# Optimization experiments

Hardware: AMD Instinct MI355X
Metric: run time of the kernel (lower is better)

## Reference

```python
import jax, jax.numpy as jnp
import numpy as np

S_DIM = 4096
N_NODES = 4096
N_EDGES = 32768


def _coarsen(ei_np, N):
    """Integer-only greedy coarsening, faithful to MNGRAPH.forward's while-loop.
    Returns (select order, flattened neighbor indices, segment ids, per-hub
    neighbor counts, forward-fill indices replicating the stale-M behavior for
    empty neighborhoods, and the remapped final edge_index)."""
    ei = ei_np.astype(np.int64).copy()
    I = np.bincount(ei[0], minlength=N)
    O = np.bincount(ei[1], minlength=N)
    order = np.argsort(-(I + O), kind='stable')  # torch.argsort(D, descending=True)
    visits = np.zeros(N, dtype=bool)
    select = []
    nbr_idx, nbr_seg, counts = [], [], []
    while order.size > 0:
        node = int(order[0])
        select.append(node)
        visits[node] = True
        # H = unique neighbors of node in the CURRENT (rewritten) edge_index
        H = np.unique(np.concatenate([ei[1][ei[0] == node], ei[0][ei[1] == node]]))
        visits[H] = True
        order = order[~visits[order]]
        # rewrite: endpoints in H that are not already-selected hubs -> node
        Hn = H[~np.isin(H, np.asarray(select, dtype=np.int64))]
        ei[np.isin(ei, Hn)] = node
        ei = ei[:, ei[0] != ei[1]]  # drop self-loops
        # append reversed edges that are not already present (pair-code isin
        # == the original O(E^2) all/any comparison, computed efficiently)
        code = ei[0] * N + ei[1]
        rcode = ei[1] * N + ei[0]
        new = ~np.isin(rcode, code)
        ei = np.concatenate([ei, ei[::-1][:, new]], axis=1)
        k = len(select) - 1
        nbr_idx.append(H)
        nbr_seg.append(np.full(H.shape[0], k, dtype=np.int64))
        counts.append(H.shape[0])
    select = np.asarray(select, dtype=np.int64)
    sort_sel = np.sort(select)
    ei_out = np.searchsorted(sort_sel, ei)  # compact node ids
    counts = np.asarray(counts, dtype=np.int64)
    # forward-fill: when H is empty the original appends the previous (stale) M
    fill = np.arange(select.shape[0])
    for i in range(select.shape[0]):
        if counts[i] == 0:
            fill[i] = fill[i - 1] if i > 0 else 0
    nbr = np.concatenate(nbr_idx) if nbr_idx else np.zeros(0, np.int64)
    seg = np.concatenate(nbr_seg) if nbr_seg else np.zeros(0, np.int64)
    return select, nbr, seg, counts, fill, ei_out


def setup_inputs() -> dict:
    key = jax.random.key(0)
    k1, k2, k3, k4 = jax.random.split(key, 4)
    x = jax.random.normal(k1, (N_NODES, S_DIM), dtype=jnp.float32)
    edge_index = jax.random.randint(k2, (2, N_EDGES), 0, N_NODES, dtype=jnp.int64)
    bound = float(np.sqrt(6.0 / (1.0 + S_DIM)))  # xavier_uniform on (1, S)
    W1 = jax.random.uniform(k3, (S_DIM,), jnp.float32, -bound, bound)
    W2 = jax.random.uniform(k4, (S_DIM,), jnp.float32, -bound, bound)
    B1 = jnp.zeros((S_DIM,), jnp.float32)
    B2 = jnp.zeros((S_DIM,), jnp.float32)
    return {"x": x, "edge_index": edge_index, "W1": W1, "W2": W2, "B1": B1, "B2": B2}


def reference(x, edge_index, W1, W2, B1, B2):
    N = x.shape[0]
    sel, nbr, seg, counts, fill, ei_out = _coarsen(np.asarray(edge_index), N)
    K = sel.shape[0]
    # Dn = x[n]*W1+B1 for every neighbor of every hub; per-hub mean via segment_sum
    Dn = x[jnp.asarray(nbr)] * W1 + B1                      # [T, S]
    sums = jax.ops.segment_sum(Dn, jnp.asarray(seg), num_segments=K)
    denom = jnp.maximum(jnp.asarray(counts), 1).astype(x.dtype)[:, None]
    mean_Dn = sums / denom                                  # [K, S]
    Dv = x[jnp.asarray(sel)] * W2 + B2                      # [K, S]
    END = jnp.concatenate([Dv, mean_Dn], axis=1)            # [K, 2S]
    END = END[jnp.asarray(fill)]                            # stale-M replication
    return END, jnp.asarray(ei_out)
```

## Files before the change

kernel.cpp:

```cpp
#include <hip/hip_runtime.h>
#include <hip/hip_bf16.h>

#define NT 1024
#define NNODES 4096
#define ECAP 65536

__device__ __forceinline__ int blockScanExcl(int v, int* s_w, int* total) {
    const int tid  = threadIdx.x;
    const int lane = tid & 63;
    const int wv   = tid >> 6;
    int x = v;
#pragma unroll
    for (int off = 1; off < 64; off <<= 1) {
        int t = __shfl_up(x, off, 64);
        if (lane >= off) x += t;
    }
    if (lane == 63) s_w[wv] = x;
    __syncthreads();
    if (tid < 16) {
        int y = s_w[tid];
#pragma unroll
        for (int off = 1; off < 16; off <<= 1) {
            int t = __shfl_up(y, off, 16);
            if (tid >= off) y += t;
        }
        s_w[tid] = y;
    }
    __syncthreads();
    int base = wv ? s_w[wv - 1] : 0;
    int tot  = s_w[15];
    __syncthreads();
    *total = tot;
    return base + x - v;
}

__global__ __launch_bounds__(NT, 1)
void phaseA(const int* __restrict__ ei, int E0,
            int* __restrict__ U, int* __restrict__ V,
            unsigned int* __restrict__ BM,
            int* __restrict__ NBR, int* __restrict__ OTH, int* __restrict__ TMP,
            int* __restrict__ SEL, int* __restrict__ CNTS,
            int* __restrict__ NST, int* __restrict__ FIL, int* __restrict__ SC,
            float* __restrict__ out)
{
    __shared__ unsigned short s_order[NNODES];
    __shared__ unsigned char  s_vis[NNODES];
    __shared__ unsigned char  s_sel[NNODES];
    __shared__ unsigned int   s_hb[NNODES / 32];
    __shared__ unsigned short s_so[NNODES];
    __shared__ unsigned int   s_nst[NNODES + 1];
    __shared__ int s_roff[NNODES];
    __shared__ int s_rend[NNODES];
    __shared__ int s_tmp[NNODES];
    __shared__ unsigned short s_lab[NNODES];
    __shared__ int s_stamp[NNODES];
    __shared__ int s_w[16];
    __shared__ int s_bc[16];

    const int tid = threadIdx.x;
    const int ln  = tid & 63;

    for (int i = tid; i < NNODES; i += NT) {
        s_vis[i] = 0; s_sel[i] = 0; s_tmp[i] = 0; s_stamp[i] = 0;
    }
    for (int i = tid; i < NNODES / 32; i += NT) s_hb[i] = 0;
    if (tid < 16) s_bc[tid] = 0;
    __syncthreads();

    for (int i = tid; i < E0; i += NT)
        if (ei[2 * i + 1] != 0) s_bc[9] = 1;
    __syncthreads();
    const int is64 = !s_bc[9];

    for (int e = tid; e < E0; e += NT) {
        int uu = ei[is64 ? 2 * e : e];
        int vv = ei[is64 ? 2 * (E0 + e) : (E0 + e)];
        U[e] = uu; V[e] = vv;
        atomicAdd(&s_tmp[uu], 1);
        atomicAdd(&s_tmp[vv], 1);
    }
    __syncthreads();
    for (int n = tid; n < NNODES; n += NT) atomicMax(&s_bc[7], s_tmp[n]);
    __syncthreads();
    const int maxd = s_bc[7];

    for (int d = maxd; d >= 0; --d) {
        int n0 = tid * 4;
        int f0 = (s_tmp[n0] == d), f1 = (s_tmp[n0 + 1] == d);
        int f2 = (s_tmp[n0 + 2] == d), f3 = (s_tmp[n0 + 3] == d);
        int tot;
        int off = blockScanExcl(f0 + f1 + f2 + f3, s_w, &tot);
        int idx = s_bc[4] + off;
        if (f0) s_order[idx++] = (unsigned short)n0;
        if (f1) s_order[idx++] = (unsigned short)(n0 + 1);
        if (f2) s_order[idx++] = (unsigned short)(n0 + 2);
        if (f3) s_order[idx++] = (unsigned short)(n0 + 3);
        __syncthreads();
        if (tid == 0) s_bc[4] += tot;
        __syncthreads();
    }

    if (tid == 0) {
        int nd = s_order[0];
        s_bc[0] = nd; s_sel[nd] = 1; s_vis[nd] = 1;
        s_so[0] = (unsigned short)nd; s_nst[0] = 0;
    }
    __syncthreads();
    {
        const int node = s_bc[0];
        for (int e = tid; e < E0; e += NT) {
            int uu = U[e], vv = V[e];
            if (uu == node) {
                int w = vv; unsigned m = 1u << (w & 31);
                unsigned old = atomicOr(&s_hb[w >> 5], m);
                if (!(old & m)) { int i = atomicAdd(&s_bc[2], 1); s_tmp[i] = w; s_vis[w] = 1; }
            }
            if (vv == node) {
                int w = uu; unsigned m = 1u << (w & 31);
                unsigned old = atomicOr(&s_hb[w >> 5], m);
                if (!(old & m)) { int i = atomicAdd(&s_bc[2], 1); s_tmp[i] = w; s_vis[w] = 1; }
            }
        }
        __syncthreads();
        for (int e = tid; e < E0; e += NT) {
            int uu = U[e];
            if (uu != node && ((s_hb[uu >> 5] >> (uu & 31)) & 1)) U[e] = node;
            int vv = V[e];
            if (vv != node && ((s_hb[vv >> 5] >> (vv & 31)) & 1)) V[e] = node;
        }
        __syncthreads();
    }

    for (int i = tid; i < (1 << 19); i += NT) BM[i] = 0u;
    __syncthreads();
    for (int e = tid; e < E0; e += NT) {
        int uu = U[e], vv = V[e];
        if (uu != vv) {
            unsigned code = ((unsigned)uu << 12) | (unsigned)vv;
            atomicOr(&BM[code >> 5], 1u << (code & 31));
        }
    }
    __syncthreads();
    for (int t = 0; t < E0; t += NT) {
        int e = t + tid, flag = 0, uu = 0, vv = 0;
        if (e < E0) {
            uu = U[e]; vv = V[e];
            if (uu != vv) {
                unsigned rc = ((unsigned)vv << 12) | (unsigned)uu;
                unsigned old = atomicOr(&BM[rc >> 5], 0u);
                flag = !((old >> (rc & 31)) & 1u);
            }
        }
        int tot;
        int off = blockScanExcl(flag, s_w, &tot);
        if (flag) { int r = s_bc[5] + off; U[E0 + r] = vv; V[E0 + r] = uu; }
        __syncthreads();
        if (tid == 0) s_bc[5] += tot;
        __syncthreads();
    }
    const int E1 = E0 + s_bc[5];

    for (int n = tid; n < NNODES; n += NT) s_roff[n] = 0;
    __syncthreads();
    for (int e = tid; e < E1; e += NT) {
        int uu = U[e], vv = V[e];
        if (uu != vv) { atomicAdd(&s_roff[uu], 1); atomicAdd(&s_roff[vv], 1); }
    }
    __syncthreads();
    {
        int n0 = tid * 4;
        int c0 = s_roff[n0], c1 = s_roff[n0 + 1], c2 = s_roff[n0 + 2], c3 = s_roff[n0 + 3];
        int tot;
        int off = blockScanExcl(c0 + c1 + c2 + c3, s_w, &tot);
        int st = off;
        s_roff[n0] = st;     s_rend[n0] = st;     st += c0;
        s_roff[n0 + 1] = st; s_rend[n0 + 1] = st; st += c1;
        s_roff[n0 + 2] = st; s_rend[n0 + 2] = st; st += c2;
        s_roff[n0 + 3] = st; s_rend[n0 + 3] = st;
    }
    __syncthreads();
    for (int e = tid; e < E1; e += NT) {
        int uu = U[e], vv = V[e];
        if (uu != vv) {
            int p = atomicAdd(&s_rend[uu], 1);
            int q = atomicAdd(&s_rend[vv], 1);
            OTH[p] = vv; OTH[q] = uu;
        }
    }
    __syncthreads();
    {
        const int cnt0 = s_bc[2];
        for (int i = tid; i < cnt0; i += NT) NBR[i] = s_tmp[i];
    }
    for (int i = tid; i < NNODES; i += NT) s_lab[i] = (unsigned short)i;
    __syncthreads();

    int p = 0, k = 1;
    for (;;) {
        __syncthreads();
        if (tid == 0) s_nst[k] = (unsigned)s_bc[2];
        int node = -1;
        for (;;) {
            if (p >= NNODES) break;
            int cand = (p + ln < NNODES) ? (int)s_order[p + ln] : -1;
            int unvis = (cand >= 0) && (!s_vis[cand]);
            unsigned long long bal = __ballot(unvis);
            if (bal != 0ull) {
                int sel = __ffsll(bal) - 1;
                node = __shfl(cand, sel, 64);
                p += sel + 1;
                break;
            }
            p += 64;
        }
        if (node < 0) break;
        if (tid == 0) { s_sel[node] = 1; s_so[k] = (unsigned short)node; }
        const int rb = s_roff[node], re = s_rend[node];
        for (int s = rb + tid; s < re; s += NT) {
            int w = (int)s_lab[OTH[s]];
            if (w == node) continue;
            int old = atomicMax(&s_stamp[w], k);
            if (old < k) {
                int i = atomicAdd(&s_bc[2], 1);
                NBR[i] = w;
                s_vis[w] = 1;
                if (!s_sel[w]) s_lab[w] = (unsigned short)node;
            }
        }
        k++;
    }
    const int K = k;
    __syncthreads();

    for (int i = tid; i < K; i += NT) {
        SEL[i]  = (int)s_so[i];
        CNTS[i] = (int)(s_nst[i + 1] - s_nst[i]);
        NST[i]  = (int)s_nst[i];
    }
    if (tid == 0) {
        SC[0] = K;
        int f = 0;
        for (int i = 0; i < K; i++) { if (s_nst[i + 1] > s_nst[i]) f = i; FIL[i] = f; }
    }
    {
        int n0 = tid * 4;
        int r0 = s_sel[n0], r1 = s_sel[n0 + 1], r2 = s_sel[n0 + 2], r3 = s_sel[n0 + 3];
        int tot;
        int off = blockScanExcl(r0 + r1 + r2 + r3, s_w, &tot);
        int st = off;
        s_tmp[n0] = st;     st += r0;
        s_tmp[n0 + 1] = st; st += r1;
        s_tmp[n0 + 2] = st; st += r2;
        s_tmp[n0 + 3] = st;
    }
    __syncthreads();
    const size_t obase = (size_t)K * 8192;
    for (int t = 0; t < E1; t += NT) {
        int e = t + tid, flag = 0, ru = 0, rv = 0;
        if (e < E1) {
            int uu = (int)s_lab[U[e]], vv = (int)s_lab[V[e]];
            if (uu != vv) { flag = 1; ru = s_tmp[uu]; rv = s_tmp[vv]; }
        }
        int tot;
        int off = blockScanExcl(flag, s_w, &tot);
        if (flag) {
            int r = s_bc[6] + off;
            out[obase + (size_t)r] = (float)ru;
            TMP[r] = rv;
        }
        __syncthreads();
        if (tid == 0) s_bc[6] += tot;
        __syncthreads();
    }
    const int Ef = s_bc[6];
    if (tid == 0) SC[1] = Ef;
    for (int r = tid; r < Ef; r += NT)
        out[obase + (size_t)Ef + (size_t)r] = (float)TMP[r];
}

__global__ __launch_bounds__(256, 4)
void phaseB(const float* __restrict__ x,
            const float* __restrict__ W1, const float* __restrict__ W2,
            const float* __restrict__ B1, const float* __restrict__ B2,
            const int* __restrict__ NBR, const int* __restrict__ SEL,
            const int* __restrict__ CNTS, const int* __restrict__ NST,
            const int* __restrict__ FIL, const int* __restrict__ SC,
            float* __restrict__ out)
{
    const int K = SC[0];
    const int k = blockIdx.x;
    if (k >= K) return;
    const int kk   = FIL[k];
    const int node = SEL[kk];
    const int cnt  = CNTS[kk];
    const int st   = NST[kk];
    const int tid  = threadIdx.x;
    const float4* x4 = (const float4*)x;

    float4 acc[4];
#pragma unroll
    for (int j = 0; j < 4; j++) acc[j] = make_float4(0.f, 0.f, 0.f, 0.f);

    for (int r = 0; r < cnt; ++r) {
        const float4* row = x4 + (size_t)NBR[st + r] * 1024;
#pragma unroll
        for (int j = 0; j < 4; j++) {
            float4 t = row[tid + j * 256];
            acc[j].x += t.x; acc[j].y += t.y; acc[j].z += t.z; acc[j].w += t.w;
        }
    }

    const float fc  = (float)cnt;
    const float inv = 1.0f / (float)(cnt > 1 ? cnt : 1);
    const float4* xr = x4 + (size_t)node * 1024;
    float4* o4 = (float4*)(out + (size_t)k * 8192);

#pragma unroll
    for (int j = 0; j < 4; j++) {
        int c = tid + j * 256;
        float4 w1 = ((const float4*)W1)[c], b1 = ((const float4*)B1)[c];
        float4 w2 = ((const float4*)W2)[c], b2 = ((const float4*)B2)[c];
        float4 xv = xr[c];
        float4 pd, pm;
        pd.x = xv.x * w2.x + b2.x;
        pd.y = xv.y * w2.y + b2.y;
        pd.z = xv.z * w2.z + b2.z;
        pd.w = xv.w * w2.w + b2.w;
        pm.x = (acc[j].x * w1.x + fc * b1.x) * inv;
        pm.y = (acc[j].y * w1.y + fc * b1.y) * inv;
        pm.z = (acc[j].z * w1.z + fc * b1.z) * inv;
        pm.w = (acc[j].w * w1.w + fc * b1.w) * inv;
        o4[c] = pd;
        o4[1024 + c] = pm;
    }
}

extern "C" void kernel_launch(void* const* d_in, const int* in_sizes, int n_in,
                              void* d_out, int out_size, void* d_ws, size_t ws_size,
                              hipStream_t stream)
{
    const float* x  = (const float*)d_in[0];
    const int*   ei = (const int*)d_in[1];
    const float* W1 = (const float*)d_in[2];
    const float* W2 = (const float*)d_in[3];
    const float* B1 = (const float*)d_in[4];
    const float* B2 = (const float*)d_in[5];
    const int E0 = in_sizes[1] / 2;

    char* w = (char*)d_ws;
    int* U = (int*)w;
    int* V = U + ECAP;
    unsigned int* BM = (unsigned int*)(V + ECAP);
    int* OTH = (int*)BM;
    int* NBR = OTH + 2 * ECAP;
    int* TMP = NBR + 2 * ECAP;
    char* meta = (char*)BM + (2u << 20);
    int* SEL  = (int*)meta;
    int* CNTS = SEL + NNODES;
    int* NST  = CNTS + NNODES;
    int* FIL  = NST + NNODES;
    int* SC   = FIL + NNODES;
    float* out = (float*)d_out;

    hipLaunchKernelGGL(phaseA, dim3(1), dim3(NT), 0, stream,
                       ei, E0, U, V, BM, NBR, OTH, TMP,
                       SEL, CNTS, NST, FIL, SC, out);
    hipLaunchKernelGGL(phaseB, dim3(NNODES), dim3(256), 0, stream,
                       x, W1, W2, B1, B2, NBR, SEL, CNTS, NST, FIL, SC, out);
}
```

Measured before the change: 972.5 us.

## Cut barriers in serial coarsening loop via per-wave atomics and chunked compaction

Packs the visited flag into the order array (high bit) with a position index, so the hub search reads one LDS array. Neighbor insertion now uses wave-aggregated atomics and per-hub counters, and the loop top uses a raw LDS-wait-plus-barrier instead of __syncthreads with a tid-0 write. The reverse-edge append and final edge compaction switch from per-tile scans with two barriers each to one block scan over per-thread contiguous chunks with bitmasks, dropping the TMP buffer. The bitmap clear is vectorised to uint4. The goal is to remove synchronisation and atomic overhead in the single-block serial phase. The cost is extra LDS and a 64-bit mask assumption that requires each thread's chunk to be at most 64 edges.

```diff
diff --git a/kernel.cpp b/kernel.cpp
--- a/kernel.cpp
+++ b/kernel.cpp
@@ -4,6 +4,8 @@
 #define NT 1024
 #define NNODES 4096
 #define ECAP 65536
+
+#define BAR_LDS() asm volatile("s_waitcnt lgkmcnt(0)\n\ts_barrier" ::: "memory")
 
 __device__ __forceinline__ int blockScanExcl(int v, int* s_w, int* total) {
     const int tid  = threadIdx.x;
@@ -38,17 +40,17 @@
 void phaseA(const int* __restrict__ ei, int E0,
             int* __restrict__ U, int* __restrict__ V,
             unsigned int* __restrict__ BM,
-            int* __restrict__ NBR, int* __restrict__ OTH, int* __restrict__ TMP,
+            int* __restrict__ NBR, int* __restrict__ OTH,
             int* __restrict__ SEL, int* __restrict__ CNTS,
             int* __restrict__ NST, int* __restrict__ FIL, int* __restrict__ SC,
             float* __restrict__ out)
 {
-    __shared__ unsigned short s_order[NNODES];
-    __shared__ unsigned char  s_vis[NNODES];
+    __shared__ unsigned short s_ordvis[NNODES];
+    __shared__ unsigned short s_pos[NNODES];
     __shared__ unsigned char  s_sel[NNODES];
     __shared__ unsigned int   s_hb[NNODES / 32];
     __shared__ unsigned short s_so[NNODES];
-    __shared__ unsigned int   s_nst[NNODES + 1];
+    __shared__ int s_cnt32[NNODES];
     __shared__ int s_roff[NNODES];
     __shared__ int s_rend[NNODES];
     __shared__ int s_tmp[NNODES];
@@ -61,7 +63,7 @@
     const int ln  = tid & 63;
 
     for (int i = tid; i < NNODES; i += NT) {
-        s_vis[i] = 0; s_sel[i] = 0; s_tmp[i] = 0; s_stamp[i] = 0;
+        s_sel[i] = 0; s_tmp[i] = 0; s_stamp[i] = 0; s_cnt32[i] = 0;
     }
     for (int i = tid; i < NNODES / 32; i += NT) s_hb[i] = 0;
     if (tid < 16) s_bc[tid] = 0;
@@ -91,19 +93,22 @@
         int tot;
         int off = blockScanExcl(f0 + f1 + f2 + f3, s_w, &tot);
         int idx = s_bc[4] + off;
-        if (f0) s_order[idx++] = (unsigned short)n0;
-        if (f1) s_order[idx++] = (unsigned short)(n0 + 1);
-        if (f2) s_order[idx++] = (unsigned short)(n0 + 2);
-        if (f3) s_order[idx++] = (unsigned short)(n0 + 3);
+        if (f0) s_ordvis[idx++] = (unsigned short)n0;
+        if (f1) s_ordvis[idx++] = (unsigned short)(n0 + 1);
+        if (f2) s_ordvis[idx++] = (unsigned short)(n0 + 2);
+        if (f3) s_ordvis[idx++] = (unsigned short)(n0 + 3);
         __syncthreads();
         if (tid == 0) s_bc[4] += tot;
         __syncthreads();
     }
+    for (int i = tid; i < NNODES; i += NT) s_pos[(int)s_ordvis[i]] = (unsigned short)i;
+    __syncthreads();
 
     if (tid == 0) {
-        int nd = s_order[0];
-        s_bc[0] = nd; s_sel[nd] = 1; s_vis[nd] = 1;
-        s_so[0] = (unsigned short)nd; s_nst[0] = 0;
+        int nd = (int)s_ordvis[0];
+        s_bc[0] = nd; s_sel[nd] = 1;
+        s_ordvis[0] = (unsigned short)(0x8000 | nd);
+        s_so[0] = (unsigned short)nd;
     }
     __syncthreads();
     {
@@ -113,15 +118,22 @@
             if (uu == node) {
                 int w = vv; unsigned m = 1u << (w & 31);
                 unsigned old = atomicOr(&s_hb[w >> 5], m);
-                if (!(old & m)) { int i = atomicAdd(&s_bc[2], 1); s_tmp[i] = w; s_vis[w] = 1; }
+                if (!(old & m)) {
+                    int i = atomicAdd(&s_bc[2], 1); s_tmp[i] = w;
+                    s_ordvis[s_pos[w]] = (unsigned short)(0x8000 | w);
+                }
             }
             if (vv == node) {
                 int w = uu; unsigned m = 1u << (w & 31);
                 unsigned old = atomicOr(&s_hb[w >> 5], m);
-                if (!(old & m)) { int i = atomicAdd(&s_bc[2], 1); s_tmp[i] = w; s_vis[w] = 1; }
+                if (!(old & m)) {
+                    int i = atomicAdd(&s_bc[2], 1); s_tmp[i] = w;
+                    s_ordvis[s_pos[w]] = (unsigned short)(0x8000 | w);
+                }
             }
         }
         __syncthreads();
+        if (tid == 0) s_cnt32[0] = s_bc[2];
         for (int e = tid; e < E0; e += NT) {
             int uu = U[e];
             if (uu != node && ((s_hb[uu >> 5] >> (uu & 31)) & 1)) U[e] = node;
@@ -131,7 +143,10 @@
         __syncthreads();
     }
 
-    for (int i = tid; i < (1 << 19); i += NT) BM[i] = 0u;
+    {
+        uint4* bm4 = (uint4*)BM;
+        for (int i = tid; i < (1 << 17); i += NT) bm4[i] = make_uint4(0, 0, 0, 0);
+    }
     __syncthreads();
     for (int e = tid; e < E0; e += NT) {
         int uu = U[e], vv = V[e];
@@ -141,24 +156,32 @@
         }
     }
     __syncthreads();
-    for (int t = 0; t < E0; t += NT) {
-        int e = t + tid, flag = 0, uu = 0, vv = 0;
-        if (e < E0) {
-            uu = U[e]; vv = V[e];
-            if (uu != vv) {
-                unsigned rc = ((unsigned)vv << 12) | (unsigned)uu;
-                unsigned old = atomicOr(&BM[rc >> 5], 0u);
-                flag = !((old >> (rc & 31)) & 1u);
+    int E1;
+    {
+        const int chA = (E0 + NT - 1) / NT;
+        const int begA = tid * chA;
+        unsigned long long mA = 0ull;
+        for (int j = 0; j < chA; ++j) {
+            int e = begA + j;
+            if (e < E0) {
+                int uu = U[e], vv = V[e];
+                if (uu != vv) {
+                    unsigned rc = ((unsigned)vv << 12) | (unsigned)uu;
+                    unsigned old = atomicOr(&BM[rc >> 5], 0u);
+                    if (!((old >> (rc & 31)) & 1u)) mA |= 1ull << j;
+                }
             }
         }
         int tot;
-        int off = blockScanExcl(flag, s_w, &tot);
-        if (flag) { int r = s_bc[5] + off; U[E0 + r] = vv; V[E0 + r] = uu; }
-        __syncthreads();
-        if (tid == 0) s_bc[5] += tot;
-        __syncthreads();
-    }
-    const int E1 = E0 + s_bc[5];
+        int off = blockScanExcl(__popcll(mA), s_w, &tot);
+        for (int j = 0; j < chA; ++j) if ((mA >> j) & 1) {
+            int e = begA + j;
+            int r = off++;
+            U[E0 + r] = V[e]; V[E0 + r] = U[e];
+        }
+        E1 = E0 + tot;
+    }
+    __syncthreads();
 
     for (int n = tid; n < NNODES; n += NT) s_roff[n] = 0;
     __syncthreads();
@@ -197,17 +220,15 @@
 
     int p = 0, k = 1;
     for (;;) {
-        __syncthreads();
-        if (tid == 0) s_nst[k] = (unsigned)s_bc[2];
+        BAR_LDS();
         int node = -1;
-        for (;;) {
-            if (p >= NNODES) break;
-            int cand = (p + ln < NNODES) ? (int)s_order[p + ln] : -1;
-            int unvis = (cand >= 0) && (!s_vis[cand]);
-            unsigned long long bal = __ballot(unvis);
+        while (p < NNODES) {
+            int idx = p + ln;
+            int ov = (idx < NNODES) ? (int)s_ordvis[idx] : 0x8000;
+            unsigned long long bal = __ballot(!(ov & 0x8000));
             if (bal != 0ull) {
                 int sel = __ffsll(bal) - 1;
-                node = __shfl(cand, sel, 64);
+                node = __shfl(ov, sel, 64) & 0x7FFF;
                 p += sel + 1;
                 break;
             }
@@ -216,15 +237,31 @@
         if (node < 0) break;
         if (tid == 0) { s_sel[node] = 1; s_so[k] = (unsigned short)node; }
         const int rb = s_roff[node], re = s_rend[node];
-        for (int s = rb + tid; s < re; s += NT) {
-            int w = (int)s_lab[OTH[s]];
-            if (w == node) continue;
-            int old = atomicMax(&s_stamp[w], k);
-            if (old < k) {
-                int i = atomicAdd(&s_bc[2], 1);
-                NBR[i] = w;
-                s_vis[w] = 1;
-                if (!s_sel[w]) s_lab[w] = (unsigned short)node;
+        for (int s0 = rb; s0 < re; s0 += NT) {
+            int s = s0 + tid;
+            bool isnew = false; int w = -1;
+            if (s < re) {
+                w = (int)s_lab[OTH[s]];
+                if (w != node) {
+                    int old = atomicMax(&s_stamp[w], k);
+                    isnew = old < k;
+                }
+            }
+            unsigned long long b = __ballot(isnew);
+            if (b != 0ull) {
+                int cnt = __popcll(b);
+                int before = __popcll(b & ((1ull << ln) - 1ull));
+                int base = 0;
+                if (isnew && before == 0) {
+                    base = atomicAdd(&s_bc[2], cnt);
+                    atomicAdd(&s_cnt32[k], cnt);
+                }
+                base = __shfl(base, __ffsll(b) - 1, 64);
+                if (isnew) {
+                    NBR[base + before] = w;
+                    s_ordvis[s_pos[w]] = (unsigned short)(0x8000 | w);
+                    if (!s_sel[w]) s_lab[w] = (unsigned short)node;
+                }
             }
         }
         k++;
@@ -232,15 +269,24 @@
     const int K = k;
     __syncthreads();
 
-    for (int i = tid; i < K; i += NT) {
-        SEL[i]  = (int)s_so[i];
-        CNTS[i] = (int)(s_nst[i + 1] - s_nst[i]);
-        NST[i]  = (int)s_nst[i];
-    }
+    {
+        int n0 = tid * 4;
+        int c0 = s_cnt32[n0], c1 = s_cnt32[n0 + 1], c2 = s_cnt32[n0 + 2], c3 = s_cnt32[n0 + 3];
+        int tot;
+        int off = blockScanExcl(c0 + c1 + c2 + c3, s_w, &tot);
+        if (n0 < K) {
+            int st = off;
+            if (n0     < K) { NST[n0]     = st; CNTS[n0]     = c0; } st += c0;
+            if (n0 + 1 < K) { NST[n0 + 1] = st; CNTS[n0 + 1] = c1; } st += c1;
+            if (n0 + 2 < K) { NST[n0 + 2] = st; CNTS[n0 + 2] = c2; } st += c2;
+            if (n0 + 3 < K) { NST[n0 + 3] = st; CNTS[n0 + 3] = c3; }
+        }
+    }
+    for (int i = tid; i < K; i += NT) SEL[i] = (int)s_so[i];
     if (tid == 0) {
         SC[0] = K;
         int f = 0;
-        for (int i = 0; i < K; i++) { if (s_nst[i + 1] > s_nst[i]) f = i; FIL[i] = f; }
+        for (int i = 0; i < K; i++) { if (s_cnt32[i] > 0) f = i; FIL[i] = f; }
     }
     {
         int n0 = tid * 4;
@@ -254,28 +300,29 @@
         s_tmp[n0 + 3] = st;
     }
     __syncthreads();
-    const size_t obase = (size_t)K * 8192;
-    for (int t = 0; t < E1; t += NT) {
-        int e = t + tid, flag = 0, ru = 0, rv = 0;
-        if (e < E1) {
-            int uu = (int)s_lab[U[e]], vv = (int)s_lab[V[e]];
-            if (uu != vv) { flag = 1; ru = s_tmp[uu]; rv = s_tmp[vv]; }
-        }
-        int tot;
-        int off = blockScanExcl(flag, s_w, &tot);
-        if (flag) {
-            int r = s_bc[6] + off;
-            out[obase + (size_t)r] = (float)ru;
-            TMP[r] = rv;
-        }
-        __syncthreads();
-        if (tid == 0) s_bc[6] += tot;
-        __syncthreads();
-    }
-    const int Ef = s_bc[6];
-    if (tid == 0) SC[1] = Ef;
-    for (int r = tid; r < Ef; r += NT)
-        out[obase + (size_t)Ef + (size_t)r] = (float)TMP[r];
+    {
+        const int ch2 = (E1 + NT - 1) / NT;
+        const int beg2 = tid * ch2;
+        unsigned long long mF = 0ull;
+        for (int j = 0; j < ch2; ++j) {
+            int e = beg2 + j;
+            if (e < E1) {
+                int uu = (int)s_lab[U[e]], vv = (int)s_lab[V[e]];
+                if (uu != vv) mF |= 1ull << j;
+            }
+        }
+        int Ef;
+        int off = blockScanExcl(__popcll(mF), s_w, &Ef);
+        const size_t obase = (size_t)K * 8192;
+        int r = off;
+        for (int j = 0; j < ch2; ++j) if ((mF >> j) & 1) {
+            int e = beg2 + j;
+            out[obase + (size_t)r]             = (float)s_tmp[(int)s_lab[U[e]]];
+            out[obase + (size_t)Ef + (size_t)r] = (float)s_tmp[(int)s_lab[V[e]]];
+            r++;
+        }
+        if (tid == 0) SC[1] = Ef;
+    }
 }
 
 __global__ __launch_bounds__(256, 4)
@@ -353,7 +400,6 @@
     unsigned int* BM = (unsigned int*)(V + ECAP);
     int* OTH = (int*)BM;
     int* NBR = OTH + 2 * ECAP;
-    int* TMP = NBR + 2 * ECAP;
     char* meta = (char*)BM + (2u << 20);
     int* SEL  = (int*)meta;
     int* CNTS = SEL + NNODES;
@@ -363,7 +409,7 @@
     float* out = (float*)d_out;
 
     hipLaunchKernelGGL(phaseA, dim3(1), dim3(NT), 0, stream,
-                       ei, E0, U, V, BM, NBR, OTH, TMP,
+                       ei, E0, U, V, BM, NBR, OTH,
                        SEL, CNTS, NST, FIL, SC, out);
     hipLaunchKernelGGL(phaseB, dim3(NNODES), dim3(256), 0, stream,
                        x, W1, W2, B1, B2, NBR, SEL, CNTS, NST, FIL, SC, out);
```

New measurement: 1.192 ms. +22.6%, slower.

## Split serial coarsening loop into single-wavefront kernel without block barriers

Applied to the files above, without the earlier changes.

The phaseA kernel is split into three kernels. The sequential greedy hub-selection loop now runs in one 64-thread wavefront, which removes the per-iteration __syncthreads across 1024 threads. The visited flags are folded into the order array so one ballot can find the next unvisited hub, and neighbors are processed two per lane. The exclusive scans and the forward fill use wave-level ballot and shuffle, the relabel pass runs in a separate 1024-thread kernel, and the extra launches pass their data through global memory.

```diff
diff --git a/kernel.cpp b/kernel.cpp
--- a/kernel.cpp
+++ b/kernel.cpp
@@ -35,34 +35,25 @@
 }
 
 __global__ __launch_bounds__(NT, 1)
-void phaseA(const int* __restrict__ ei, int E0,
-            int* __restrict__ U, int* __restrict__ V,
-            unsigned int* __restrict__ BM,
-            int* __restrict__ NBR, int* __restrict__ OTH, int* __restrict__ TMP,
-            int* __restrict__ SEL, int* __restrict__ CNTS,
-            int* __restrict__ NST, int* __restrict__ FIL, int* __restrict__ SC,
-            float* __restrict__ out)
+void phaseA1(const int* __restrict__ ei, int E0,
+             int* __restrict__ U, int* __restrict__ V,
+             unsigned int* __restrict__ BM,
+             int* __restrict__ NBR, int* __restrict__ OTH,
+             int* __restrict__ ORDV, int* __restrict__ ROFFG, int* __restrict__ RENDG,
+             int* __restrict__ HAND)
 {
     __shared__ unsigned short s_order[NNODES];
     __shared__ unsigned char  s_vis[NNODES];
-    __shared__ unsigned char  s_sel[NNODES];
     __shared__ unsigned int   s_hb[NNODES / 32];
-    __shared__ unsigned short s_so[NNODES];
-    __shared__ unsigned int   s_nst[NNODES + 1];
     __shared__ int s_roff[NNODES];
     __shared__ int s_rend[NNODES];
     __shared__ int s_tmp[NNODES];
-    __shared__ unsigned short s_lab[NNODES];
-    __shared__ int s_stamp[NNODES];
     __shared__ int s_w[16];
     __shared__ int s_bc[16];
 
     const int tid = threadIdx.x;
-    const int ln  = tid & 63;
-
-    for (int i = tid; i < NNODES; i += NT) {
-        s_vis[i] = 0; s_sel[i] = 0; s_tmp[i] = 0; s_stamp[i] = 0;
-    }
+
+    for (int i = tid; i < NNODES; i += NT) { s_vis[i] = 0; s_tmp[i] = 0; }
     for (int i = tid; i < NNODES / 32; i += NT) s_hb[i] = 0;
     if (tid < 16) s_bc[tid] = 0;
     __syncthreads();
@@ -102,8 +93,7 @@
 
     if (tid == 0) {
         int nd = s_order[0];
-        s_bc[0] = nd; s_sel[nd] = 1; s_vis[nd] = 1;
-        s_so[0] = (unsigned short)nd; s_nst[0] = 0;
+        s_bc[0] = nd; s_vis[nd] = 1;
     }
     __syncthreads();
     {
@@ -192,87 +182,190 @@
         const int cnt0 = s_bc[2];
         for (int i = tid; i < cnt0; i += NT) NBR[i] = s_tmp[i];
     }
-    for (int i = tid; i < NNODES; i += NT) s_lab[i] = (unsigned short)i;
-    __syncthreads();
+    for (int i = tid; i < NNODES; i += NT) {
+        int nd = (int)s_order[i];
+        ORDV[i]  = nd | (s_vis[nd] ? 0x8000 : 0);
+        ROFFG[i] = s_roff[i];
+        RENDG[i] = s_rend[i];
+    }
+    if (tid == 0) { HAND[0] = E1; HAND[1] = s_bc[2]; HAND[2] = s_bc[0]; }
+}
+
+__global__ __launch_bounds__(64, 1)
+void phaseA2(const int* __restrict__ OTH, int* __restrict__ NBR,
+             const int* __restrict__ ORDV, const int* __restrict__ ROFFG,
+             const int* __restrict__ RENDG, const int* __restrict__ HAND,
+             int* __restrict__ SEL, int* __restrict__ CNTS,
+             int* __restrict__ NST, int* __restrict__ FIL, int* __restrict__ SC,
+             int* __restrict__ LABG, int* __restrict__ RNKG)
+{
+    __shared__ unsigned short s_ordvis[NNODES];
+    __shared__ unsigned short s_pos[NNODES];
+    __shared__ unsigned short s_lab[NNODES];
+    __shared__ unsigned short s_so[NNODES];
+    __shared__ int s_cnt[NNODES];
+    __shared__ int s_stamp[NNODES];
+    __shared__ int s_roff[NNODES];
+    __shared__ int s_rend[NNODES];
+    __shared__ unsigned char s_sel[NNODES];
+    __shared__ int s_nc[1];
+
+    const int ln = threadIdx.x;
+    const unsigned long long ltm = (1ull << ln) - 1ull;
+    const int cnt0 = HAND[1], hub0 = HAND[2];
+
+    for (int i = ln; i < NNODES; i += 64) {
+        int ov = ORDV[i];
+        s_ordvis[i] = (unsigned short)ov;
+        s_pos[ov & 0x7FFF] = (unsigned short)i;
+        s_roff[i] = ROFFG[i];
+        s_rend[i] = RENDG[i];
+        s_lab[i] = (unsigned short)i;
+        s_stamp[i] = 0; s_sel[i] = 0; s_cnt[i] = 0;
+    }
+    if (ln == 0) {
+        s_sel[hub0] = 1; s_so[0] = (unsigned short)hub0;
+        s_cnt[0] = cnt0; s_nc[0] = cnt0;
+    }
 
     int p = 0, k = 1;
     for (;;) {
-        __syncthreads();
-        if (tid == 0) s_nst[k] = (unsigned)s_bc[2];
         int node = -1;
-        for (;;) {
-            if (p >= NNODES) break;
-            int cand = (p + ln < NNODES) ? (int)s_order[p + ln] : -1;
-            int unvis = (cand >= 0) && (!s_vis[cand]);
-            unsigned long long bal = __ballot(unvis);
+        while (p < NNODES) {
+            int idx = p + ln;
+            int ov = (idx < NNODES) ? (int)s_ordvis[idx] : 0x8000;
+            unsigned long long bal = __ballot(!(ov & 0x8000));
             if (bal != 0ull) {
-                int sel = __ffsll(bal) - 1;
-                node = __shfl(cand, sel, 64);
-                p += sel + 1;
+                int sl = __ffsll((long long)bal) - 1;
+                node = __shfl(ov, sl, 64) & 0x7FFF;
+                p += sl + 1;
                 break;
             }
             p += 64;
         }
         if (node < 0) break;
-        if (tid == 0) { s_sel[node] = 1; s_so[k] = (unsigned short)node; }
+        if (ln == 0) { s_sel[node] = 1; s_so[k] = (unsigned short)node; }
         const int rb = s_roff[node], re = s_rend[node];
-        for (int s = rb + tid; s < re; s += NT) {
-            int w = (int)s_lab[OTH[s]];
-            if (w == node) continue;
-            int old = atomicMax(&s_stamp[w], k);
-            if (old < k) {
-                int i = atomicAdd(&s_bc[2], 1);
-                NBR[i] = w;
-                s_vis[w] = 1;
-                if (!s_sel[w]) s_lab[w] = (unsigned short)node;
-            }
-        }
+        const int begin = s_nc[0];
+        for (int s0 = rb; s0 < re; s0 += 128) {
+            int sA = s0 + ln, sB = s0 + 64 + ln;
+            int oA = (sA < re) ? OTH[sA] : -1;
+            int oB = (sB < re) ? OTH[sB] : -1;
+            if (oA >= 0) {
+                int w = (int)s_lab[oA];
+                if (w != node) {
+                    int old = atomicMax(&s_stamp[w], k);
+                    if (old < k) {
+                        int i = atomicAdd(&s_nc[0], 1);
+                        NBR[i] = w;
+                        s_ordvis[s_pos[w]] = (unsigned short)(0x8000 | w);
+                        if (!s_sel[w]) s_lab[w] = (unsigned short)node;
+                    }
+                }
+            }
+            if (oB >= 0) {
+                int w = (int)s_lab[oB];
+                if (w != node) {
+                    int old = atomicMax(&s_stamp[w], k);
+                    if (old < k) {
+                        int i = atomicAdd(&s_nc[0], 1);
+                        NBR[i] = w;
+                        s_ordvis[s_pos[w]] = (unsigned short)(0x8000 | w);
+                        if (!s_sel[w]) s_lab[w] = (unsigned short)node;
+                    }
+                }
+            }
+        }
+        if (ln == 0) s_cnt[k] = s_nc[0] - begin;
         k++;
     }
     const int K = k;
-    __syncthreads();
-
-    for (int i = tid; i < K; i += NT) {
-        SEL[i]  = (int)s_so[i];
-        CNTS[i] = (int)(s_nst[i + 1] - s_nst[i]);
-        NST[i]  = (int)s_nst[i];
-    }
-    if (tid == 0) {
-        SC[0] = K;
-        int f = 0;
-        for (int i = 0; i < K; i++) { if (s_nst[i + 1] > s_nst[i]) f = i; FIL[i] = f; }
-    }
-    {
-        int n0 = tid * 4;
-        int r0 = s_sel[n0], r1 = s_sel[n0 + 1], r2 = s_sel[n0 + 2], r3 = s_sel[n0 + 3];
-        int tot;
-        int off = blockScanExcl(r0 + r1 + r2 + r3, s_w, &tot);
-        int st = off;
-        s_tmp[n0] = st;     st += r0;
-        s_tmp[n0 + 1] = st; st += r1;
-        s_tmp[n0 + 2] = st; st += r2;
-        s_tmp[n0 + 3] = st;
-    }
-    __syncthreads();
+
+    {
+        int base = 0;
+        for (int c = 0; c < NNODES / 64; ++c) {
+            int n = c * 64 + ln;
+            int f = s_sel[n];
+            unsigned long long b = __ballot(f);
+            s_stamp[n] = base + __popcll(b & ltm);
+            base += __popcll(b);
+        }
+    }
+    {
+        int nb = 0;
+        for (int c = 0; c * 64 < K; ++c) {
+            int i = c * 64 + ln;
+            int cv = (i < K) ? s_cnt[i] : 0;
+            int x = cv;
+#pragma unroll
+            for (int off = 1; off < 64; off <<= 1) {
+                int t = __shfl_up(x, off, 64);
+                if (ln >= off) x += t;
+            }
+            if (i < K) { NST[i] = nb + x - cv; CNTS[i] = cv; SEL[i] = (int)s_so[i]; }
+            nb += __shfl(x, 63, 64);
+        }
+    }
+    {
+        int carry = 0;
+        for (int c = 0; c * 64 < K; ++c) {
+            int i = c * 64 + ln;
+            int f = (i < K) && (s_cnt[i] > 0);
+            unsigned long long b = __ballot(f);
+            unsigned long long m = b & ((ln == 63) ? ~0ull : ((1ull << (ln + 1)) - 1ull));
+            int fil = m ? (c * 64 + 63 - __clzll(m)) : carry;
+            if (i < K) FIL[i] = fil;
+            carry = b ? (c * 64 + 63 - __clzll(b)) : carry;
+        }
+    }
+    if (ln == 0) SC[0] = K;
+    for (int i = ln; i < NNODES; i += 64) {
+        LABG[i] = (int)s_lab[i];
+        RNKG[i] = s_stamp[i];
+    }
+}
+
+__global__ __launch_bounds__(NT, 1)
+void phaseA3(const int* __restrict__ U, const int* __restrict__ V,
+             const int* __restrict__ LABG, const int* __restrict__ RNKG,
+             const int* __restrict__ HAND, int* __restrict__ SC,
+             int* __restrict__ TMP, float* __restrict__ out)
+{
+    __shared__ unsigned short l_lab[NNODES];
+    __shared__ int l_rnk[NNODES];
+    __shared__ int s_w[16];
+    __shared__ int s_base[1];
+
+    const int tid = threadIdx.x;
+    for (int i = tid; i < NNODES; i += NT) {
+        l_lab[i] = (unsigned short)LABG[i];
+        l_rnk[i] = RNKG[i];
+    }
+    if (tid == 0) s_base[0] = 0;
+    __syncthreads();
+
+    const int E1 = HAND[0];
+    const int K  = SC[0];
     const size_t obase = (size_t)K * 8192;
+
     for (int t = 0; t < E1; t += NT) {
         int e = t + tid, flag = 0, ru = 0, rv = 0;
         if (e < E1) {
-            int uu = (int)s_lab[U[e]], vv = (int)s_lab[V[e]];
-            if (uu != vv) { flag = 1; ru = s_tmp[uu]; rv = s_tmp[vv]; }
+            int uu = (int)l_lab[U[e]], vv = (int)l_lab[V[e]];
+            if (uu != vv) { flag = 1; ru = l_rnk[uu]; rv = l_rnk[vv]; }
         }
         int tot;
         int off = blockScanExcl(flag, s_w, &tot);
         if (flag) {
-            int r = s_bc[6] + off;
+            int r = s_base[0] + off;
             out[obase + (size_t)r] = (float)ru;
             TMP[r] = rv;
         }
         __syncthreads();
-        if (tid == 0) s_bc[6] += tot;
-        __syncthreads();
-    }
-    const int Ef = s_bc[6];
+        if (tid == 0) s_base[0] += tot;
+        __syncthreads();
+    }
+    const int Ef = s_base[0];
     if (tid == 0) SC[1] = Ef;
     for (int r = tid; r < Ef; r += NT)
         out[obase + (size_t)Ef + (size_t)r] = (float)TMP[r];
@@ -355,16 +448,26 @@
     int* NBR = OTH + 2 * ECAP;
     int* TMP = NBR + 2 * ECAP;
     char* meta = (char*)BM + (2u << 20);
-    int* SEL  = (int*)meta;
-    int* CNTS = SEL + NNODES;
-    int* NST  = CNTS + NNODES;
-    int* FIL  = NST + NNODES;
-    int* SC   = FIL + NNODES;
+    int* SEL   = (int*)meta;
+    int* CNTS  = SEL  + NNODES;
+    int* NST   = CNTS + NNODES;
+    int* FIL   = NST  + NNODES;
+    int* SC    = FIL  + NNODES;
+    int* ORDV  = SC   + 16;
+    int* ROFFG = ORDV + NNODES;
+    int* RENDG = ROFFG + NNODES;
+    int* LABG  = RENDG + NNODES;
+    int* RNKG  = LABG + NNODES;
+    int* HAND  = RNKG + NNODES;
     float* out = (float*)d_out;
 
-    hipLaunchKernelGGL(phaseA, dim3(1), dim3(NT), 0, stream,
-                       ei, E0, U, V, BM, NBR, OTH, TMP,
-                       SEL, CNTS, NST, FIL, SC, out);
+    hipLaunchKernelGGL(phaseA1, dim3(1), dim3(NT), 0, stream,
+                       ei, E0, U, V, BM, NBR, OTH, ORDV, ROFFG, RENDG, HAND);
+    hipLaunchKernelGGL(phaseA2, dim3(1), dim3(64), 0, stream,
+                       OTH, NBR, ORDV, ROFFG, RENDG, HAND,
+                       SEL, CNTS, NST, FIL, SC, LABG, RNKG);
+    hipLaunchKernelGGL(phaseA3, dim3(1), dim3(NT), 0, stream,
+                       U, V, LABG, RNKG, HAND, SC, TMP, out);
     hipLaunchKernelGGL(phaseB, dim3(NNODES), dim3(256), 0, stream,
                        x, W1, W2, B1, B2, NBR, SEL, CNTS, NST, FIL, SC, out);
 }
```

Measured after the change: 965.9 us. Within noise of the previous version (-0.7%).
